# Performance work log

Measured on AMD Instinct MI355X. Metric: run time of the kernel, lower is better.

## Reference

```python
import jax, jax.numpy as jnp
import numpy as np

N_NODES = 40000
N_EDGES = 640000
C = 128        # in_channels == hidden_channels
H = 8          # heads
D = C // H     # head dim = 16
L = 2          # num HGTConv layers
OUT = 64       # final fc out_channels


def _segment_softmax(logits, seg, num_segments):
    # logits: [E, H], seg: [E] destination ids
    m = jax.ops.segment_max(logits, seg, num_segments=num_segments)
    m = jnp.where(jnp.isfinite(m), m, 0.0)  # empty segments -> 0
    e = jnp.exp(logits - m[seg])
    s = jax.ops.segment_sum(e, seg, num_segments=num_segments)
    return e / (s[seg] + 1e-16)


def setup_inputs() -> dict:
    key = jax.random.key(0)
    ks = jax.random.split(key, 20)
    p = lambda k, shape, s=0.05: (jax.random.normal(k, shape, jnp.float32) * s)
    x = jax.random.normal(ks[0], (N_NODES, C), jnp.float32)
    edge_index = jax.random.randint(ks[1], (2, N_EDGES), 0, N_NODES, jnp.int64)
    return {
        "x": x,
        "edge_index": edge_index,
        # per-layer stacked params (all layers have C->C dims)
        "Wk": p(ks[2], (L, C, C)), "bk": jnp.zeros((L, C), jnp.float32),
        "Wq": p(ks[3], (L, C, C)), "bq": jnp.zeros((L, C), jnp.float32),
        "Wv": p(ks[4], (L, C, C)), "bv": jnp.zeros((L, C), jnp.float32),
        "a_rel": p(ks[5], (L, H, D, D), 0.1),  # relation key transform
        "m_rel": p(ks[6], (L, H, D, D), 0.1),  # relation message transform
        "p_rel": jnp.ones((L, H), jnp.float32),  # relation prior per head
        "skip": jnp.ones((L,), jnp.float32),      # skip gate logits
        "aW": p(ks[7], (L, C, C)), "ab": jnp.zeros((L, C), jnp.float32),
        "fcW": p(ks[8], (C, OUT)), "fcb": jnp.zeros((OUT,), jnp.float32),
    }


def reference(x, edge_index, Wk, bk, Wq, bq, Wv, bv, a_rel, m_rel, p_rel, skip,
              aW, ab, fcW, fcb):
    src, dst = edge_index[0], edge_index[1]
    n = x.shape[0]
    n_layers, heads, d = a_rel.shape[0], a_rel.shape[1], a_rel.shape[2]
    inv_sqrt_d = 1.0 / np.sqrt(d).astype(np.float32)

    h = x
    for l in range(n_layers):
        k = (h @ Wk[l] + bk[l]).reshape(n, heads, d)
        q = (h @ Wq[l] + bq[l]).reshape(n, heads, d)
        v = (h @ Wv[l] + bv[l]).reshape(n, heads, d)
        # relation-specific transforms applied at node level (single edge type)
        k2 = jnp.einsum('nhd,hde->nhe', k, a_rel[l])
        v2 = jnp.einsum('nhd,hde->nhe', v, m_rel[l])
        # per-edge attention logits [E, H]
        logits = jnp.sum(q[dst] * k2[src], axis=-1) * p_rel[l] * inv_sqrt_d
        alpha = _segment_softmax(logits, dst, n)                 # [E, H]
        msg = v2[src] * alpha[:, :, None]                        # [E, H, D]
        agg = jax.ops.segment_sum(msg, dst, num_segments=n)      # [N, H, D]
        agg = agg.reshape(n, heads * d)
        a = jax.nn.gelu(agg) @ aW[l] + ab[l]
        beta = jax.nn.sigmoid(skip[l])
        h = beta * a + (1.0 - beta) * h     # HGT skip (dims match)
        h = jax.nn.relu(h)                  # model-level relu
    return h @ fcW + fcb
```

## Files before the change

### kernel.cpp

```cpp
#include <hip/hip_runtime.h>
#include <hip/hip_bf16.h>
#include <math.h>

#define NN 40000
#define NE 640000

typedef __attribute__((ext_vector_type(8))) short short8;
typedef __attribute__((ext_vector_type(8))) unsigned short u16x8;
typedef __attribute__((ext_vector_type(4))) float f32x4;
typedef _Float16 h16x2 __attribute__((ext_vector_type(2)));

#define WBLOCKS 547
#define GBLOCKS 625
#define NCO 157
#define P1B 160
#define EPB 4000
#define NH (NCO*P1B)
#define NHB 99

#if __has_builtin(__builtin_amdgcn_fdot2)
#define HAS_FDOT2 1
#else
#define HAS_FDOT2 0
#endif

__device__ __forceinline__ float gelu_tanh(float x) {
    float x3 = x * x * x;
    float u = 0.7978845608028654f * (x + 0.044715f * x3);
    return 0.5f * x * (1.0f + tanhf(u));
}

__device__ __forceinline__ unsigned short f2bf(float v) {
    __hip_bfloat16 h = __float2bfloat16(v);
    return *reinterpret_cast<unsigned short*>(&h);
}

__device__ __forceinline__ unsigned short f2h(float v) {
    union { _Float16 h; unsigned short u; } c;
    c.h = (_Float16)v;
    return c.u;
}

__device__ __forceinline__ float bf2f(unsigned short u) {
    union { unsigned int i; float f; } c;
    c.i = ((unsigned int)u) << 16;
    return c.f;
}

__device__ __forceinline__ void unpack8(u16x8 u, float* f) {
    union { u16x8 v; unsigned int d[4]; } c; c.v = u;
    #pragma unroll
    for (int i = 0; i < 4; ++i) {
        union { unsigned int i_; float f_; } lo, hi;
        lo.i_ = c.d[i] << 16;
        hi.i_ = c.d[i] & 0xffff0000u;
        f[2 * i] = lo.f_;
        f[2 * i + 1] = hi.f_;
    }
}

union kv8 { u16x8 u; h16x2 p[4]; _Float16 h[8]; };
union frag8 { short8 s; unsigned short u[8]; u16x8 v; };

__global__ __launch_bounds__(256) void prep_kernel(
    const float* __restrict__ Wq, const float* __restrict__ bq,
    const float* __restrict__ Wk, const float* __restrict__ bk,
    const float* __restrict__ a_rel,
    const float* __restrict__ Wv, const float* __restrict__ bv,
    const float* __restrict__ m_rel,
    const float* __restrict__ p_rel,
    const float* __restrict__ aW, const float* __restrict__ fcW,
    unsigned short* __restrict__ BfT, float* __restrict__ biasf,
    unsigned short* __restrict__ aWT, unsigned short* __restrict__ fcWT,
    const int* __restrict__ eidx, int* __restrict__ Hmat)
{
    if (blockIdx.x >= WBLOCKS) {
        __shared__ int chist[NCO];
        int b = blockIdx.x - WBLOCKS;
        int t = threadIdx.x;
        if (t < NCO) chist[t] = 0;
        __syncthreads();
        int base = b * EPB;
        for (int e = base + t; e < base + EPB; e += 256)
            atomicAdd(&chist[eidx[NE + e] >> 8], 1);
        __syncthreads();
        if (t < NCO) Hmat[t * P1B + b] = chist[t];
        return;
    }
    int idx = blockIdx.x * 256 + threadIdx.x;
    if (idx < 2 * 129 * 384) {
        int l = idx / (129 * 384);
        int j = idx - l * (129 * 384);
        int r = j / 384;
        int col = j - r * 384;
        const float* Wq_l = Wq + l * 16384;
        const float* Wk_l = Wk + l * 16384;
        const float* Wv_l = Wv + l * 16384;
        const float* ar_l = a_rel + l * 2048;
        const float* mr_l = m_rel + l * 2048;
        float val;
        if (col < 128) {
            val = (r < 128) ? Wq_l[r * 128 + col] : bq[l * 128 + col];
        } else if (col < 256) {
            int cc = col - 128; int h = cc >> 4; int eo = cc & 15;
            float scale = p_rel[l * 8 + h] * 0.25f * 1.4426950408889634f;
            float s = 0.f;
            #pragma unroll
            for (int d = 0; d < 16; ++d) {
                float w = (r < 128) ? Wk_l[r * 128 + h * 16 + d] : bk[l * 128 + h * 16 + d];
                s += w * ar_l[h * 256 + d * 16 + eo];
            }
            val = s * scale;
        } else {
            int cc = col - 256; int h = cc >> 4; int eo = cc & 15;
            float s = 0.f;
            #pragma unroll
            for (int d = 0; d < 16; ++d) {
                float w = (r < 128) ? Wv_l[r * 128 + h * 16 + d] : bv[l * 128 + h * 16 + d];
                s += w * mr_l[h * 256 + d * 16 + eo];
            }
            val = s;
        }
        if (r < 128) BfT[(size_t)l * 49152 + (size_t)col * 128 + r] = f2bf(val);
        else         biasf[l * 384 + col] = val;
    } else if (idx < 2 * 129 * 384 + 2 * 16384) {
        int i = idx - 2 * 129 * 384;
        int l = i >> 14; int j = i & 16383;
        int r = j >> 7, c = j & 127;
        aWT[(size_t)l * 16384 + (size_t)c * 128 + r] = f2bf(aW[(size_t)l * 16384 + r * 128 + c]);
    } else {
        int i = idx - (2 * 129 * 384 + 2 * 16384);
        int c = i >> 7, r = i & 127;
        fcWT[(size_t)c * 128 + r] = f2bf(fcW[(size_t)r * 64 + c]);
    }
}

__global__ __launch_bounds__(256) void scan_blocks_kernel(
    const int* __restrict__ in, int* __restrict__ out, int* __restrict__ bsum)
{
    __shared__ int s[256];
    int t = threadIdx.x;
    int i = blockIdx.x * 256 + t;
    int v = (i < NH) ? in[i] : 0;
    s[t] = v;
    __syncthreads();
    #pragma unroll
    for (int off = 1; off < 256; off <<= 1) {
        int u = (t >= off) ? s[t - off] : 0;
        __syncthreads();
        s[t] += u;
        __syncthreads();
    }
    if (i < NH) out[i] = s[t] - v;
    if (t == 255) bsum[blockIdx.x] = s[255];
}

__global__ __launch_bounds__(256) void scan_top_kernel(
    const int* __restrict__ bsum, int* __restrict__ boffs)
{
    __shared__ int s[256];
    int t = threadIdx.x;
    int v = (t < NHB) ? bsum[t] : 0;
    s[t] = v;
    __syncthreads();
    #pragma unroll
    for (int off = 1; off < 256; off <<= 1) {
        int u = (t >= off) ? s[t - off] : 0;
        __syncthreads();
        s[t] += u;
        __syncthreads();
    }
    boffs[t] = s[t] - v;
}

__global__ __launch_bounds__(256) void scan_add_kernel(
    int* __restrict__ out, const int* __restrict__ boffs)
{
    int i = blockIdx.x * 256 + threadIdx.x;
    if (i < NH) out[i] += boffs[blockIdx.x];
}

__global__ __launch_bounds__(256) void pass2_kernel(
    const int* __restrict__ eidx, const int* __restrict__ O, int* __restrict__ ebuk)
{
    __shared__ int cur[NCO];
    int b = blockIdx.x, t = threadIdx.x;
    if (t < NCO) cur[t] = O[t * P1B + b];
    __syncthreads();
    int base = b * EPB;
    for (int e = base + t; e < base + EPB; e += 256) {
        int s = eidx[e];
        int d = eidx[NE + e];
        int pos = atomicAdd(&cur[d >> 8], 1);
        ebuk[pos] = ((d & 255) << 16) | s;
    }
}

__global__ __launch_bounds__(256) void qkv0_p3_kernel(
    const float* __restrict__ Af, const unsigned short* __restrict__ BT,
    const float* __restrict__ bias,
    unsigned short* __restrict__ qb, unsigned short* __restrict__ kvb,
    const int* __restrict__ O, const int* __restrict__ ebuk,
    int* __restrict__ deg, int* __restrict__ offs, int* __restrict__ srcSorted)
{
    if (blockIdx.x >= GBLOCKS) {
        __shared__ int hist[256], loffs[256], cur[256];
        int c = blockIdx.x - GBLOCKS;
        int t = threadIdx.x;
        int base = O[c * P1B];
        int end = (c < NCO - 1) ? O[(c + 1) * P1B] : NE;
        hist[t] = 0;
        __syncthreads();
        for (int i = base + t; i < end; i += 256)
            atomicAdd(&hist[ebuk[i] >> 16], 1);
        __syncthreads();
        int v = hist[t];
        loffs[t] = v;
        __syncthreads();
        #pragma unroll
        for (int off = 1; off < 256; off <<= 1) {
            int u = (t >= off) ? loffs[t - off] : 0;
            __syncthreads();
            loffs[t] += u;
            __syncthreads();
        }
        int excl = loffs[t] - v;
        int n = c * 256 + t;
        if (n < NN) { deg[n] = v; offs[n] = base + excl; }
        cur[t] = excl;
        __syncthreads();
        for (int i = base + t; i < end; i += 256) {
            int p = ebuk[i];
            int pos = atomicAdd(&cur[p >> 16], 1);
            srcSorted[base + pos] = p & 0xffff;
        }
        return;
    }
    __shared__ unsigned short Bs[64][136];
    int t = threadIdx.x;
    int row0 = blockIdx.x * 64;
    int w = t >> 6;
    int lr = t & 15;
    int quad = (t & 63) >> 4;
    int row = row0 + w * 16 + lr;

    frag8 af[4];
    {
        const float* ap = Af + (size_t)row * 128 + quad * 8;
        #pragma unroll
        for (int kc = 0; kc < 4; ++kc) {
            float4 a0 = *(const float4*)(ap + kc * 32);
            float4 a1 = *(const float4*)(ap + kc * 32 + 4);
            af[kc].u[0] = f2bf(a0.x); af[kc].u[1] = f2bf(a0.y);
            af[kc].u[2] = f2bf(a0.z); af[kc].u[3] = f2bf(a0.w);
            af[kc].u[4] = f2bf(a1.x); af[kc].u[5] = f2bf(a1.y);
            af[kc].u[6] = f2bf(a1.z); af[kc].u[7] = f2bf(a1.w);
        }
    }

    #pragma unroll
    for (int ct = 0; ct < 6; ++ct) {
        if (ct) __syncthreads();
        #pragma unroll
        for (int i = 0; i < 4; ++i) {
            int idx = t + i * 256;
            int r = idx >> 4;
            int c8 = (idx & 15) * 8;
            *(u16x8*)(&Bs[r][c8]) = *(const u16x8*)(BT + (size_t)(ct * 64 + r) * 128 + c8);
        }
        __syncthreads();
        f32x4 acc[4] = {{0.f,0.f,0.f,0.f},{0.f,0.f,0.f,0.f},
                        {0.f,0.f,0.f,0.f},{0.f,0.f,0.f,0.f}};
        #pragma unroll
        for (int kc = 0; kc < 4; ++kc) {
            #pragma unroll
            for (int n4 = 0; n4 < 4; ++n4) {
                short8 bfr = *(const short8*)(&Bs[n4 * 16 + lr][kc * 32 + quad * 8]);
                acc[n4] = __builtin_amdgcn_mfma_f32_16x16x32_bf16(bfr, af[kc].s, acc[n4], 0, 0, 0);
            }
        }
        unsigned short* dst = (ct < 2) ? (qb + (size_t)row * 128 + (ct & 1) * 64)
                                       : (kvb + (size_t)row * 256 + (ct - 2) * 64);
        #pragma unroll
        for (int n4 = 0; n4 < 4; ++n4) {
            int colb = n4 * 16 + quad * 4;
            float4 bv = *(const float4*)(bias + ct * 64 + colb);
            ushort4 o;
            if (ct >= 4) {
                o.x = f2bf(acc[n4][0] + bv.x);
                o.y = f2bf(acc[n4][1] + bv.y);
                o.z = f2bf(acc[n4][2] + bv.z);
                o.w = f2bf(acc[n4][3] + bv.w);
            } else {
                o.x = f2h(acc[n4][0] + bv.x);
                o.y = f2h(acc[n4][1] + bv.y);
                o.z = f2h(acc[n4][2] + bv.z);
                o.w = f2h(acc[n4][3] + bv.w);
            }
            *(ushort4*)(dst + colb) = o;
        }
    }
}

template <int HPFMT, int P2>
__global__ __launch_bounds__(256) void fused_kernel(
    const unsigned short* __restrict__ aggb,
    const unsigned short* __restrict__ aWT, const float* __restrict__ ab,
    const float* __restrict__ skip_p,
    const float* __restrict__ HprevF, const unsigned short* __restrict__ HprevB,
    unsigned short* __restrict__ hb_out,
    const unsigned short* __restrict__ W2T, const float* __restrict__ bias2,
    unsigned short* __restrict__ qb, unsigned short* __restrict__ kvb,
    float* __restrict__ outF)
{
    __shared__ unsigned short As[64][136];
    __shared__ unsigned short Bs[64][136];
    int t = threadIdx.x;
    int row0 = blockIdx.x * 64;
    int w = t >> 6;
    int lr = t & 15;
    int quad = (t & 63) >> 4;
    int row = row0 + w * 16 + lr;

    frag8 agf[4];
    {
        const unsigned short* ap = aggb + (size_t)row * 128 + quad * 8;
        #pragma unroll
        for (int kc = 0; kc < 4; ++kc) {
            u16x8 u = *(const u16x8*)(ap + kc * 32);
            #pragma unroll
            for (int j = 0; j < 8; ++j) agf[kc].u[j] = f2bf(gelu_tanh(bf2f(u[j])));
        }
    }

    float sv = skip_p[0];
    float beta = 1.f / (1.f + expf(-sv));
    float omb = 1.f - beta;

    f32x4 hacc[2][4];
    #pragma unroll
    for (int ct = 0; ct < 2; ++ct) {
        if (ct) __syncthreads();
        #pragma unroll
        for (int i = 0; i < 4; ++i) {
            int idx = t + i * 256;
            int r = idx >> 4;
            int c8 = (idx & 15) * 8;
            *(u16x8*)(&Bs[r][c8]) = *(const u16x8*)(aWT + (size_t)(ct * 64 + r) * 128 + c8);
        }
        __syncthreads();
        #pragma unroll
        for (int n4 = 0; n4 < 4; ++n4) hacc[ct][n4] = (f32x4){0.f,0.f,0.f,0.f};
        #pragma unroll
        for (int kc = 0; kc < 4; ++kc) {
            #pragma unroll
            for (int n4 = 0; n4 < 4; ++n4) {
                short8 bfr = *(const short8*)(&Bs[n4 * 16 + lr][kc * 32 + quad * 8]);
                hacc[ct][n4] = __builtin_amdgcn_mfma_f32_16x16x32_bf16(bfr, agf[kc].s, hacc[ct][n4], 0, 0, 0);
            }
        }
    }

    #pragma unroll
    for (int ct = 0; ct < 2; ++ct) {
        #pragma unroll
        for (int n4 = 0; n4 < 4; ++n4) {
            int colb = ct * 64 + n4 * 16 + quad * 4;
            float4 bv = *(const float4*)(ab + colb);
            float hp[4];
            if (HPFMT == 0) {
                float4 h4 = *(const float4*)(HprevF + (size_t)row * 128 + colb);
                hp[0] = h4.x; hp[1] = h4.y; hp[2] = h4.z; hp[3] = h4.w;
            } else {
                ushort4 h4 = *(const ushort4*)(HprevB + (size_t)row * 128 + colb);
                hp[0] = bf2f(h4.x); hp[1] = bf2f(h4.y); hp[2] = bf2f(h4.z); hp[3] = bf2f(h4.w);
            }
            ushort4 o;
            o.x = f2bf(fmaxf(beta * (hacc[ct][n4][0] + bv.x) + omb * hp[0], 0.f));
            o.y = f2bf(fmaxf(beta * (hacc[ct][n4][1] + bv.y) + omb * hp[1], 0.f));
            o.z = f2bf(fmaxf(beta * (hacc[ct][n4][2] + bv.z) + omb * hp[2], 0.f));
            o.w = f2bf(fmaxf(beta * (hacc[ct][n4][3] + bv.w) + omb * hp[3], 0.f));
            *(ushort4*)(&As[w * 16 + lr][colb]) = o;
            if (P2 == 0) *(ushort4*)(hb_out + (size_t)row * 128 + colb) = o;
        }
    }
    __syncthreads();

    if (P2 == 0) {
        #pragma unroll
        for (int ct = 0; ct < 6; ++ct) {
            if (ct) __syncthreads();
            #pragma unroll
            for (int i = 0; i < 4; ++i) {
                int idx = t + i * 256;
                int r = idx >> 4;
                int c8 = (idx & 15) * 8;
                *(u16x8*)(&Bs[r][c8]) = *(const u16x8*)(W2T + (size_t)(ct * 64 + r) * 128 + c8);
            }
            __syncthreads();
            f32x4 acc[4] = {{0.f,0.f,0.f,0.f},{0.f,0.f,0.f,0.f},
                            {0.f,0.f,0.f,0.f},{0.f,0.f,0.f,0.f}};
            #pragma unroll
            for (int kc = 0; kc < 4; ++kc) {
                short8 afr = *(const short8*)(&As[w * 16 + lr][kc * 32 + quad * 8]);
                #pragma unroll
                for (int n4 = 0; n4 < 4; ++n4) {
                    short8 bfr = *(const short8*)(&Bs[n4 * 16 + lr][kc * 32 + quad * 8]);
                    acc[n4] = __builtin_amdgcn_mfma_f32_16x16x32_bf16(bfr, afr, acc[n4], 0, 0, 0);
                }
            }
            unsigned short* dst = (ct < 2) ? (qb + (size_t)row * 128 + (ct & 1) * 64)
                                           : (kvb + (size_t)row * 256 + (ct - 2) * 64);
            #pragma unroll
            for (int n4 = 0; n4 < 4; ++n4) {
                int colb = n4 * 16 + quad * 4;
                float4 bv = *(const float4*)(bias2 + ct * 64 + colb);
                ushort4 o;
                if (ct >= 4) {
                    o.x = f2bf(acc[n4][0] + bv.x);
                    o.y = f2bf(acc[n4][1] + bv.y);
                    o.z = f2bf(acc[n4][2] + bv.z);
                    o.w = f2bf(acc[n4][3] + bv.w);
                } else {
                    o.x = f2h(acc[n4][0] + bv.x);
                    o.y = f2h(acc[n4][1] + bv.y);
                    o.z = f2h(acc[n4][2] + bv.z);
                    o.w = f2h(acc[n4][3] + bv.w);
                }
                *(ushort4*)(dst + colb) = o;
            }
        }
    } else {
        #pragma unroll
        for (int i = 0; i < 4; ++i) {
            int idx = t + i * 256;
            int r = idx >> 4;
            int c8 = (idx & 15) * 8;
            *(u16x8*)(&Bs[r][c8]) = *(const u16x8*)(W2T + (size_t)r * 128 + c8);
        }
        __syncthreads();
        f32x4 acc[4] = {{0.f,0.f,0.f,0.f},{0.f,0.f,0.f,0.f},
                        {0.f,0.f,0.f,0.f},{0.f,0.f,0.f,0.f}};
        #pragma unroll
        for (int kc = 0; kc < 4; ++kc) {
            short8 afr = *(const short8*)(&As[w * 16 + lr][kc * 32 + quad * 8]);
            #pragma unroll
            for (int n4 = 0; n4 < 4; ++n4) {
                short8 bfr = *(const short8*)(&Bs[n4 * 16 + lr][kc * 32 + quad * 8]);
                acc[n4] = __builtin_amdgcn_mfma_f32_16x16x32_bf16(bfr, afr, acc[n4], 0, 0, 0);
            }
        }
        #pragma unroll
        for (int n4 = 0; n4 < 4; ++n4) {
            int colb = n4 * 16 + quad * 4;
            float4 bv = *(const float4*)(bias2 + colb);
            float4 o;
            o.x = acc[n4][0] + bv.x;
            o.y = acc[n4][1] + bv.y;
            o.z = acc[n4][2] + bv.z;
            o.w = acc[n4][3] + bv.w;
            *(float4*)(outF + (size_t)row * 64 + colb) = o;
        }
    }
}

__global__ __launch_bounds__(256) void aggregate_kernel(
    const unsigned short* __restrict__ qb, const unsigned short* __restrict__ kvb,
    const int* __restrict__ deg, const int* __restrict__ offs,
    const int* __restrict__ srcSorted, unsigned short* __restrict__ aggb)
{
    int n = (blockIdx.x * 256 + threadIdx.x) >> 6;
    int lane = threadIdx.x & 63;
    int es = lane >> 3;
    int h = lane & 7;

#if HAS_FDOT2
    h16x2 q2[8];
    {
        const h16x2* qp = (const h16x2*)(qb + (size_t)n * 128 + h * 16);
        #pragma unroll
        for (int j = 0; j < 8; ++j) q2[j] = qp[j];
    }
#else
    float q[16];
    {
        kv8 a, b;
        a.u = *(const u16x8*)(qb + (size_t)n * 128 + h * 16);
        b.u = *(const u16x8*)(qb + (size_t)n * 128 + h * 16 + 8);
        #pragma unroll
        for (int j = 0; j < 8; ++j) { q[j] = (float)a.h[j]; q[8 + j] = (float)b.h[j]; }
    }
#endif
    float acc[16];
    #pragma unroll
    for (int j = 0; j < 16; ++j) acc[j] = 0.f;
    float den = 0.f;

    int start = offs[n];
    int d = deg[n];
    if (d > 0) {
        int ng = (d + 7) >> 3;
        int lastIdx = start + d - 1;

        kv8 ka0, ka1; u16x8 vA0, vA1;
        kv8 kB0, kB1; u16x8 vB0, vB1;
        {
            int i0 = start + es; if (i0 > lastIdx) i0 = lastIdx;
            const unsigned short* p = kvb + (size_t)srcSorted[i0] * 256 + h * 16;
            ka0.u = *(const u16x8*)p;        ka1.u = *(const u16x8*)(p + 8);
            vA0 = *(const u16x8*)(p + 128);  vA1 = *(const u16x8*)(p + 136);
        }
        kB0 = ka0; kB1 = ka1; vB0 = vA0; vB1 = vA1;
        if (ng > 1) {
            int i1 = start + 8 + es; if (i1 > lastIdx) i1 = lastIdx;
            const unsigned short* p = kvb + (size_t)srcSorted[i1] * 256 + h * 16;
            kB0.u = *(const u16x8*)p;        kB1.u = *(const u16x8*)(p + 8);
            vB0 = *(const u16x8*)(p + 128);  vB1 = *(const u16x8*)(p + 136);
        }

        for (int g = 0; g < ng; ++g) {
            kv8 kC0 = ka0, kC1 = ka1; u16x8 vC0 = vA0, vC1 = vA1;
            if (g + 2 < ng) {
                int ni = start + (g + 2) * 8 + es; if (ni > lastIdx) ni = lastIdx;
                const unsigned short* p = kvb + (size_t)srcSorted[ni] * 256 + h * 16;
                kC0.u = *(const u16x8*)p;        kC1.u = *(const u16x8*)(p + 8);
                vC0 = *(const u16x8*)(p + 128);  vC1 = *(const u16x8*)(p + 136);
            }
            float pdot = 0.f;
#if HAS_FDOT2
            #pragma unroll
            for (int j = 0; j < 4; ++j) pdot = __builtin_amdgcn_fdot2(ka0.p[j], q2[j], pdot, false);
            #pragma unroll
            for (int j = 0; j < 4; ++j) pdot = __builtin_amdgcn_fdot2(ka1.p[j], q2[4 + j], pdot, false);
#else
            #pragma unroll
            for (int j = 0; j < 8; ++j) pdot = fmaf((float)ka0.h[j], q[j], pdot);
            #pragma unroll
            for (int j = 0; j < 8; ++j) pdot = fmaf((float)ka1.h[j], q[8 + j], pdot);
#endif
            float ev = (g * 8 + es < d) ? exp2f(pdot) : 0.f;
            den += ev;
            float vf[16];
            unpack8(vA0, vf); unpack8(vA1, vf + 8);
            #pragma unroll
            for (int j = 0; j < 16; ++j) acc[j] = fmaf(vf[j], ev, acc[j]);
            ka0 = kB0; ka1 = kB1; vA0 = vB0; vA1 = vB1;
            kB0 = kC0; kB1 = kC1; vB0 = vC0; vB1 = vC1;
        }
    }
    #pragma unroll
    for (int m = 8; m < 64; m <<= 1) {
        den += __shfl_xor(den, m, 64);
        #pragma unroll
        for (int j = 0; j < 16; ++j) acc[j] += __shfl_xor(acc[j], m, 64);
    }
    if (es == 0) {
        float w = 1.f / (den + 1e-16f);
        u16x8 o0, o1;
        #pragma unroll
        for (int j = 0; j < 8; ++j) {
            o0[j] = f2bf(acc[j] * w);
            o1[j] = f2bf(acc[j + 8] * w);
        }
        *(u16x8*)(aggb + (size_t)n * 128 + h * 16) = o0;
        *(u16x8*)(aggb + (size_t)n * 128 + h * 16 + 8) = o1;
    }
}

extern "C" void kernel_launch(void* const* d_in, const int* in_sizes, int n_in,
                              void* d_out, int out_size, void* d_ws, size_t ws_size,
                              hipStream_t stream) {
    const float* x     = (const float*)d_in[0];
    const int*   eidx  = (const int*)d_in[1];
    const float* Wk    = (const float*)d_in[2];
    const float* bk    = (const float*)d_in[3];
    const float* Wq    = (const float*)d_in[4];
    const float* bq    = (const float*)d_in[5];
    const float* Wv    = (const float*)d_in[6];
    const float* bv    = (const float*)d_in[7];
    const float* a_rel = (const float*)d_in[8];
    const float* m_rel = (const float*)d_in[9];
    const float* p_rel = (const float*)d_in[10];
    const float* skip  = (const float*)d_in[11];
    const float* aW    = (const float*)d_in[12];
    const float* ab    = (const float*)d_in[13];
    const float* fcW   = (const float*)d_in[14];
    const float* fcb   = (const float*)d_in[15];
    float* out = (float*)d_out;

    float* biasf = (float*)d_ws;
    unsigned short* hb   = (unsigned short*)(biasf + 768);
    unsigned short* qb   = hb + (size_t)NN * 128;
    unsigned short* kvb  = qb + (size_t)NN * 128;
    unsigned short* aggb = kvb + (size_t)NN * 256;
    unsigned short* BfT  = aggb + (size_t)NN * 128;
    unsigned short* aWT  = BfT + 2 * 384 * 128;
    unsigned short* fcWT = aWT + 2 * 128 * 128;
    int* deg       = (int*)(fcWT + 64 * 128);
    int* offs      = deg + NN;
    int* Hmat      = offs + NN;
    int* bsum      = Hmat + NH;
    int* boffs     = bsum + 256;
    int* Oarr      = boffs + 256;
    int* ebuk      = Oarr + NH;
    int* srcSorted = ebuk + NE;

    prep_kernel<<<WBLOCKS + P1B, 256, 0, stream>>>(
        Wq, bq, Wk, bk, a_rel, Wv, bv, m_rel, p_rel, aW, fcW,
        BfT, biasf, aWT, fcWT, eidx, Hmat);
    scan_blocks_kernel<<<NHB, 256, 0, stream>>>(Hmat, Oarr, bsum);
    scan_top_kernel<<<1, 256, 0, stream>>>(bsum, boffs);
    scan_add_kernel<<<NHB, 256, 0, stream>>>(Oarr, boffs);
    pass2_kernel<<<P1B, 256, 0, stream>>>(eidx, Oarr, ebuk);

    qkv0_p3_kernel<<<GBLOCKS + NCO, 256, 0, stream>>>(
        x, BfT, biasf, qb, kvb, Oarr, ebuk, deg, offs, srcSorted);
    aggregate_kernel<<<NN / 4, 256, 0, stream>>>(qb, kvb, deg, offs, srcSorted, aggb);

    fused_kernel<0, 0><<<GBLOCKS, 256, 0, stream>>>(
        aggb, aWT, ab, skip, x, nullptr, hb,
        BfT + 49152, biasf + 384, qb, kvb, nullptr);
    aggregate_kernel<<<NN / 4, 256, 0, stream>>>(qb, kvb, deg, offs, srcSorted, aggb);

    fused_kernel<1, 2><<<GBLOCKS, 256, 0, stream>>>(
        aggb, aWT + 16384, ab + 128, skip + 1, nullptr, hb, nullptr,
        fcWT, fcb, nullptr, nullptr, out);
}
```

Measured before the change: 267.4 us.

## Store K/V in FP8 and use fast exp2-based GELU tanh

Converts the per-node key and value buffers from fp16/bf16 to FP8 (e4m3) using hardware pack/unpack conversions, halving the bytes gathered per edge in the aggregation kernel. The dot product now runs in fp32 after unpacking instead of using fdot2. GELU's tanh is replaced by an exp2-based formula. FP8 storage lowers key/value precision considerably, which risks accuracy, and the extra conversion ALU work in the edge loop may offset part of the bandwidth saving.

Result: faster. 244.3 us (-8.7%).

```diff
diff --git a/kernel.cpp b/kernel.cpp
--- a/kernel.cpp
+++ b/kernel.cpp
@@ -8,6 +8,7 @@
 typedef __attribute__((ext_vector_type(8))) short short8;
 typedef __attribute__((ext_vector_type(8))) unsigned short u16x8;
 typedef __attribute__((ext_vector_type(4))) float f32x4;
+typedef __attribute__((ext_vector_type(2))) float f32v2;
 typedef _Float16 h16x2 __attribute__((ext_vector_type(2)));
 
 #define WBLOCKS 547
@@ -18,16 +19,25 @@
 #define NH (NCO*P1B)
 #define NHB 99
 
-#if __has_builtin(__builtin_amdgcn_fdot2)
-#define HAS_FDOT2 1
+#if __has_builtin(__builtin_amdgcn_cvt_pk_f32_fp8) && __has_builtin(__builtin_amdgcn_cvt_pk_fp8_f32)
+#define HAS_FP8CVT 1
 #else
-#define HAS_FDOT2 0
+#define HAS_FP8CVT 0
 #endif
+
+__device__ __forceinline__ float fast_exp2(float x) {
+#if __has_builtin(__builtin_amdgcn_exp2f)
+    return __builtin_amdgcn_exp2f(x);
+#else
+    return exp2f(x);
+#endif
+}
 
 __device__ __forceinline__ float gelu_tanh(float x) {
     float x3 = x * x * x;
     float u = 0.7978845608028654f * (x + 0.044715f * x3);
-    return 0.5f * x * (1.0f + tanhf(u));
+    float t = 1.0f - 2.0f / (1.0f + fast_exp2(2.885390081777927f * u));
+    return 0.5f * x * (1.0f + t);
 }
 
 __device__ __forceinline__ unsigned short f2bf(float v) {
@@ -47,17 +57,54 @@
     return c.f;
 }
 
-__device__ __forceinline__ void unpack8(u16x8 u, float* f) {
-    union { u16x8 v; unsigned int d[4]; } c; c.v = u;
-    #pragma unroll
-    for (int i = 0; i < 4; ++i) {
-        union { unsigned int i_; float f_; } lo, hi;
-        lo.i_ = c.d[i] << 16;
-        hi.i_ = c.d[i] & 0xffff0000u;
-        f[2 * i] = lo.f_;
-        f[2 * i + 1] = hi.f_;
-    }
-}
+#if HAS_FP8CVT
+__device__ __forceinline__ unsigned int f32x4_to_fp8(float a, float b, float c, float d) {
+    int r = 0;
+    r = __builtin_amdgcn_cvt_pk_fp8_f32(a, b, r, false);
+    r = __builtin_amdgcn_cvt_pk_fp8_f32(c, d, r, true);
+    return (unsigned int)r;
+}
+__device__ __forceinline__ void fp8x4_to_f32(unsigned int w, float* o) {
+    f32v2 lo = __builtin_amdgcn_cvt_pk_f32_fp8((int)w, false);
+    f32v2 hi = __builtin_amdgcn_cvt_pk_f32_fp8((int)w, true);
+    o[0] = lo[0]; o[1] = lo[1]; o[2] = hi[0]; o[3] = hi[1];
+}
+#else
+__device__ __forceinline__ unsigned char f2fp8_sw(float x) {
+    union { float f; unsigned u; } c; c.f = x;
+    unsigned sgn = (c.u >> 31) << 7;
+    c.u &= 0x7fffffffu;
+    if (!(c.f < 464.f)) return (unsigned char)(sgn | 0x7e);
+    if (c.f < 0.0009765625f) return (unsigned char)sgn;
+    if (c.f < 0.015625f) {
+        int q = (int)rintf(c.f * 512.f);
+        if (q > 7) return (unsigned char)(sgn | 0x08);
+        return (unsigned char)(sgn | q);
+    }
+    unsigned u = c.u;
+    unsigned lsb = (u >> 20) & 1;
+    u += 0x7ffffu + lsb;
+    int e8 = (int)(u >> 23) - 127 + 7;
+    if (e8 > 15) return (unsigned char)(sgn | 0x7e);
+    unsigned m = (u >> 20) & 7;
+    return (unsigned char)(sgn | (e8 << 3) | m);
+}
+__device__ __forceinline__ float fp8_to_f32_sw(unsigned char b) {
+    int e = (b >> 3) & 15, m = b & 7;
+    float v = (e == 0) ? ldexpf((float)m, -9) : ldexpf(8.0f + (float)m, e - 10);
+    return (b & 0x80) ? -v : v;
+}
+__device__ __forceinline__ unsigned int f32x4_to_fp8(float a, float b, float c, float d) {
+    return (unsigned int)f2fp8_sw(a) | ((unsigned int)f2fp8_sw(b) << 8) |
+           ((unsigned int)f2fp8_sw(c) << 16) | ((unsigned int)f2fp8_sw(d) << 24);
+}
+__device__ __forceinline__ void fp8x4_to_f32(unsigned int w, float* o) {
+    o[0] = fp8_to_f32_sw((unsigned char)(w & 0xff));
+    o[1] = fp8_to_f32_sw((unsigned char)((w >> 8) & 0xff));
+    o[2] = fp8_to_f32_sw((unsigned char)((w >> 16) & 0xff));
+    o[3] = fp8_to_f32_sw((unsigned char)((w >> 24) & 0xff));
+}
+#endif
 
 union kv8 { u16x8 u; h16x2 p[4]; _Float16 h[8]; };
 union frag8 { short8 s; unsigned short u[8]; u16x8 v; };
@@ -199,7 +246,7 @@
 __global__ __launch_bounds__(256) void qkv0_p3_kernel(
     const float* __restrict__ Af, const unsigned short* __restrict__ BT,
     const float* __restrict__ bias,
-    unsigned short* __restrict__ qb, unsigned short* __restrict__ kvb,
+    unsigned short* __restrict__ qb, unsigned char* __restrict__ kvb,
     const int* __restrict__ O, const int* __restrict__ ebuk,
     int* __restrict__ deg, int* __restrict__ offs, int* __restrict__ srcSorted)
 {
@@ -279,25 +326,29 @@
                 acc[n4] = __builtin_amdgcn_mfma_f32_16x16x32_bf16(bfr, af[kc].s, acc[n4], 0, 0, 0);
             }
         }
-        unsigned short* dst = (ct < 2) ? (qb + (size_t)row * 128 + (ct & 1) * 64)
-                                       : (kvb + (size_t)row * 256 + (ct - 2) * 64);
-        #pragma unroll
-        for (int n4 = 0; n4 < 4; ++n4) {
-            int colb = n4 * 16 + quad * 4;
-            float4 bv = *(const float4*)(bias + ct * 64 + colb);
-            ushort4 o;
-            if (ct >= 4) {
-                o.x = f2bf(acc[n4][0] + bv.x);
-                o.y = f2bf(acc[n4][1] + bv.y);
-                o.z = f2bf(acc[n4][2] + bv.z);
-                o.w = f2bf(acc[n4][3] + bv.w);
-            } else {
+        if (ct < 2) {
+            unsigned short* dst = qb + (size_t)row * 128 + ct * 64;
+            #pragma unroll
+            for (int n4 = 0; n4 < 4; ++n4) {
+                int colb = n4 * 16 + quad * 4;
+                float4 bv = *(const float4*)(bias + ct * 64 + colb);
+                ushort4 o;
                 o.x = f2h(acc[n4][0] + bv.x);
                 o.y = f2h(acc[n4][1] + bv.y);
                 o.z = f2h(acc[n4][2] + bv.z);
                 o.w = f2h(acc[n4][3] + bv.w);
-            }
-            *(ushort4*)(dst + colb) = o;
+                *(ushort4*)(dst + colb) = o;
+            }
+        } else {
+            unsigned char* dst = kvb + (size_t)row * 256 + (ct - 2) * 64;
+            #pragma unroll
+            for (int n4 = 0; n4 < 4; ++n4) {
+                int colb = n4 * 16 + quad * 4;
+                float4 bv = *(const float4*)(bias + ct * 64 + colb);
+                *(unsigned int*)(dst + colb) = f32x4_to_fp8(
+                    acc[n4][0] + bv.x, acc[n4][1] + bv.y,
+                    acc[n4][2] + bv.z, acc[n4][3] + bv.w);
+            }
         }
     }
 }
@@ -310,7 +361,7 @@
     const float* __restrict__ HprevF, const unsigned short* __restrict__ HprevB,
     unsigned short* __restrict__ hb_out,
     const unsigned short* __restrict__ W2T, const float* __restrict__ bias2,
-    unsigned short* __restrict__ qb, unsigned short* __restrict__ kvb,
+    unsigned short* __restrict__ qb, unsigned char* __restrict__ kvb,
     float* __restrict__ outF)
 {
     __shared__ unsigned short As[64][136];
@@ -409,25 +460,29 @@
                     acc[n4] = __builtin_amdgcn_mfma_f32_16x16x32_bf16(bfr, afr, acc[n4], 0, 0, 0);
                 }
             }
-            unsigned short* dst = (ct < 2) ? (qb + (size_t)row * 128 + (ct & 1) * 64)
-                                           : (kvb + (size_t)row * 256 + (ct - 2) * 64);
-            #pragma unroll
-            for (int n4 = 0; n4 < 4; ++n4) {
-                int colb = n4 * 16 + quad * 4;
-                float4 bv = *(const float4*)(bias2 + ct * 64 + colb);
-                ushort4 o;
-                if (ct >= 4) {
-                    o.x = f2bf(acc[n4][0] + bv.x);
-                    o.y = f2bf(acc[n4][1] + bv.y);
-                    o.z = f2bf(acc[n4][2] + bv.z);
-                    o.w = f2bf(acc[n4][3] + bv.w);
-                } else {
+            if (ct < 2) {
+                unsigned short* dst = qb + (size_t)row * 128 + ct * 64;
+                #pragma unroll
+                for (int n4 = 0; n4 < 4; ++n4) {
+                    int colb = n4 * 16 + quad * 4;
+                    float4 bv = *(const float4*)(bias2 + ct * 64 + colb);
+                    ushort4 o;
                     o.x = f2h(acc[n4][0] + bv.x);
                     o.y = f2h(acc[n4][1] + bv.y);
                     o.z = f2h(acc[n4][2] + bv.z);
                     o.w = f2h(acc[n4][3] + bv.w);
+                    *(ushort4*)(dst + colb) = o;
                 }
-                *(ushort4*)(dst + colb) = o;
+            } else {
+                unsigned char* dst = kvb + (size_t)row * 256 + (ct - 2) * 64;
+                #pragma unroll
+                for (int n4 = 0; n4 < 4; ++n4) {
+                    int colb = n4 * 16 + quad * 4;
+                    float4 bv = *(const float4*)(bias2 + ct * 64 + colb);
+                    *(unsigned int*)(dst + colb) = f32x4_to_fp8(
+                        acc[n4][0] + bv.x, acc[n4][1] + bv.y,
+                        acc[n4][2] + bv.z, acc[n4][3] + bv.w);
+                }
             }
         }
     } else {
@@ -465,7 +520,7 @@
 }
 
 __global__ __launch_bounds__(256) void aggregate_kernel(
-    const unsigned short* __restrict__ qb, const unsigned short* __restrict__ kvb,
+    const unsigned short* __restrict__ qb, const unsigned char* __restrict__ kvb,
     const int* __restrict__ deg, const int* __restrict__ offs,
     const int* __restrict__ srcSorted, unsigned short* __restrict__ aggb)
 {
@@ -474,23 +529,14 @@
     int es = lane >> 3;
     int h = lane & 7;
 
-#if HAS_FDOT2
-    h16x2 q2[8];
-    {
-        const h16x2* qp = (const h16x2*)(qb + (size_t)n * 128 + h * 16);
-        #pragma unroll
-        for (int j = 0; j < 8; ++j) q2[j] = qp[j];
-    }
-#else
-    float q[16];
+    float qf[16];
     {
         kv8 a, b;
         a.u = *(const u16x8*)(qb + (size_t)n * 128 + h * 16);
         b.u = *(const u16x8*)(qb + (size_t)n * 128 + h * 16 + 8);
         #pragma unroll
-        for (int j = 0; j < 8; ++j) { q[j] = (float)a.h[j]; q[8 + j] = (float)b.h[j]; }
-    }
-#endif
+        for (int j = 0; j < 8; ++j) { qf[j] = (float)a.h[j]; qf[8 + j] = (float)b.h[j]; }
+    }
     float acc[16];
     #pragma unroll
     for (int j = 0; j < 16; ++j) acc[j] = 0.f;
@@ -502,50 +548,52 @@
         int ng = (d + 7) >> 3;
         int lastIdx = start + d - 1;
 
-        kv8 ka0, ka1; u16x8 vA0, vA1;
-        kv8 kB0, kB1; u16x8 vB0, vB1;
+        int4 kA, vA, kB, vB;
         {
             int i0 = start + es; if (i0 > lastIdx) i0 = lastIdx;
-            const unsigned short* p = kvb + (size_t)srcSorted[i0] * 256 + h * 16;
-            ka0.u = *(const u16x8*)p;        ka1.u = *(const u16x8*)(p + 8);
-            vA0 = *(const u16x8*)(p + 128);  vA1 = *(const u16x8*)(p + 136);
-        }
-        kB0 = ka0; kB1 = ka1; vB0 = vA0; vB1 = vA1;
+            const unsigned char* p = kvb + (size_t)srcSorted[i0] * 256 + h * 16;
+            kA = *(const int4*)p;
+            vA = *(const int4*)(p + 128);
+        }
+        kB = kA; vB = vA;
         if (ng > 1) {
             int i1 = start + 8 + es; if (i1 > lastIdx) i1 = lastIdx;
-            const unsigned short* p = kvb + (size_t)srcSorted[i1] * 256 + h * 16;
-            kB0.u = *(const u16x8*)p;        kB1.u = *(const u16x8*)(p + 8);
-            vB0 = *(const u16x8*)(p + 128);  vB1 = *(const u16x8*)(p + 136);
+            const unsigned char* p = kvb + (size_t)srcSorted[i1] * 256 + h * 16;
+            kB = *(const int4*)p;
+            vB = *(const int4*)(p + 128);
         }
 
         for (int g = 0; g < ng; ++g) {
-            kv8 kC0 = ka0, kC1 = ka1; u16x8 vC0 = vA0, vC1 = vA1;
+            int4 kC = kA, vC = vA;
             if (g + 2 < ng) {
                 int ni = start + (g + 2) * 8 + es; if (ni > lastIdx) ni = lastIdx;
-                const unsigned short* p = kvb + (size_t)srcSorted[ni] * 256 + h * 16;
-                kC0.u = *(const u16x8*)p;        kC1.u = *(const u16x8*)(p + 8);
-                vC0 = *(const u16x8*)(p + 128);  vC1 = *(const u16x8*)(p + 136);
+                const unsigned char* p = kvb + (size_t)srcSorted[ni] * 256 + h * 16;
+                kC = *(const int4*)p;
+                vC = *(const int4*)(p + 128);
             }
             float pdot = 0.f;
-#if HAS_FDOT2
-            #pragma unroll
-            for (int j = 0; j < 4; ++j) pdot = __builtin_amdgcn_fdot2(ka0.p[j], q2[j], pdot, false);
-            #pragma unroll
-            for (int j = 0; j < 4; ++j) pdot = __builtin_amdgcn_fdot2(ka1.p[j], q2[4 + j], pdot, false);
-#else
-            #pragma unroll
-            for (int j = 0; j < 8; ++j) pdot = fmaf((float)ka0.h[j], q[j], pdot);
-            #pragma unroll
-            for (int j = 0; j < 8; ++j) pdot = fmaf((float)ka1.h[j], q[8 + j], pdot);
-#endif
-            float ev = (g * 8 + es < d) ? exp2f(pdot) : 0.f;
+            {
+                float kf[16];
+                fp8x4_to_f32((unsigned int)kA.x, kf);
+                fp8x4_to_f32((unsigned int)kA.y, kf + 4);
+                fp8x4_to_f32((unsigned int)kA.z, kf + 8);
+                fp8x4_to_f32((unsigned int)kA.w, kf + 12);
+                #pragma unroll
+                for (int j = 0; j < 16; ++j) pdot = fmaf(kf[j], qf[j], pdot);
+            }
+            float ev = (g * 8 + es < d) ? fast_exp2(pdot) : 0.f;
             den += ev;
-            float vf[16];
-            unpack8(vA0, vf); unpack8(vA1, vf + 8);
-            #pragma unroll
-            for (int j = 0; j < 16; ++j) acc[j] = fmaf(vf[j], ev, acc[j]);
-            ka0 = kB0; ka1 = kB1; vA0 = vB0; vA1 = vB1;
-            kB0 = kC0; kB1 = kC1; vB0 = vC0; vB1 = vC1;
+            {
+                float vf[16];
+                fp8x4_to_f32((unsigned int)vA.x, vf);
+                fp8x4_to_f32((unsigned int)vA.y, vf + 4);
+                fp8x4_to_f32((unsigned int)vA.z, vf + 8);
+                fp8x4_to_f32((unsigned int)vA.w, vf + 12);
+                #pragma unroll
+                for (int j = 0; j < 16; ++j) acc[j] = fmaf(vf[j], ev, acc[j]);
+            }
+            kA = kB; vA = vB;
+            kB = kC; vB = vC;
         }
     }
     #pragma unroll
@@ -591,8 +639,8 @@
     float* biasf = (float*)d_ws;
     unsigned short* hb   = (unsigned short*)(biasf + 768);
     unsigned short* qb   = hb + (size_t)NN * 128;
-    unsigned short* kvb  = qb + (size_t)NN * 128;
-    unsigned short* aggb = kvb + (size_t)NN * 256;
+    unsigned char*  kvb  = (unsigned char*)(qb + (size_t)NN * 128);
+    unsigned short* aggb = (unsigned short*)(kvb + (size_t)NN * 256);
     unsigned short* BfT  = aggb + (size_t)NN * 128;
     unsigned short* aWT  = BfT + 2 * 384 * 128;
     unsigned short* fcWT = aWT + 2 * 128 * 128;
```
